# Kernel optimization log

Measured on AMD Instinct MI355X. Metric: run time of the kernel, lower is better.

Reference implementation:

```python
import jax, jax.numpy as jnp
import numpy as np

N, C, HEADS = 32768, 512, 8
CK = CV = C // 2   # key/value channels (= hidden//2 per AE.block1)
F2 = C // 2        # CAM in_features
BN_EPS = 1e-5


def _bn(x, p):
    # eval-mode BatchNorm2d on [n, c, w] (h=1 squeezed); p = [gamma, beta, mean, var] each [c]
    g, b, m, v = p
    inv = g / jnp.sqrt(v + BN_EPS)
    return (x - m[None, :, None]) * inv[None, :, None] + b[None, :, None]


def _conv(x, w):
    # 1x1 Conv2d (no bias) on [n, c, w]; w: [out_c, in_c]
    return jnp.einsum('ncw,oc->now', x, w)


def _block(x, y, ea_wk, ea_bk, ea_wq, ea_bq, ea_wv, ea_bv, ea_wr, ea_br,
           pool_w1, pool_bn1, pool_w2, pool_bn2,
           adapt_w1, adapt_bn1, adapt_w2, adapt_bn2,
           delta_w1, delta_bn1, delta_w2):
    # torch: input_ = stack([x, y]).permute([0,2,1]).unsqueeze(2) -> [2, C, 1, N]; we drop h=1 -> [2, C, N]
    inp = jnp.stack([x, y]).transpose(0, 2, 1)  # [2, C, N]

    # ---------------- EfficientAttention ----------------
    keys = _conv(inp, ea_wk) + ea_bk[None, :, None]      # [2, CK, N]
    queries = _conv(inp, ea_wq) + ea_bq[None, :, None]   # [2, CK, N]
    values = _conv(inp, ea_wv) + ea_bv[None, :, None]    # [2, CV, N]
    hk, hv = CK // HEADS, CV // HEADS
    K = jax.nn.softmax(keys.reshape(2, HEADS, hk, N), axis=-1)     # softmax over positions
    Q = jax.nn.softmax(queries.reshape(2, HEADS, hk, N), axis=2)   # softmax over head channels
    V = values.reshape(2, HEADS, hv, N)
    ctx = jnp.einsum('nhkw,nhvw->nhkv', K, V)                      # [2, H, hk, hv]
    att = jnp.einsum('nhkv,nhkw->nhvw', ctx, Q).reshape(2, CV, N)  # [2, CV, N]
    ea_full = _conv(att, ea_wr) + ea_br[None, :, None] + inp       # reprojection + residual
    ea_out = ((ea_full[0] + ea_full[1]) * 0.5).T                   # [N, C]

    # ---------------- CAM ----------------
    high = inp.mean(axis=2, keepdims=True)                 # AdaptiveAvgPool2d(1) -> [2, C, 1]
    high = _bn(_conv(high, pool_w1), pool_bn1)
    high = _bn(_conv(high, pool_w2), pool_bn2)             # [2, F2, 1]
    low = _bn(_conv(inp, adapt_w1), adapt_bn1)
    low = _bn(_conv(low, adapt_w2), adapt_bn2)             # [2, F2, N]
    # bilinear upsample of a 1x1 map == broadcast
    high_up = jnp.broadcast_to(high, (2, F2, N))
    concat = jnp.concatenate([low, high_up], axis=1)       # [2, 2*F2, N]
    d = _bn(_conv(concat, delta_w1), delta_bn1)
    delta = _conv(d, delta_w2)                             # [2, 2, N]: (dx, dy)
    # grid_sample of 1x1 `high`, zeros padding, align_corners=False; norm = [w/s, h/s] = [1, 1]
    gx = jnp.linspace(-1.0, 1.0, N)[None, :] + delta[:, 0]  # h_list + delta_x, [2, N]
    gy = -1.0 + delta[:, 1]                                 # linspace(-1,1,1) = -1
    ix, iy = gx * 0.5, gy * 0.5                             # unnormalized coords for W=H=1
    wgt = jnp.clip(1.0 - jnp.abs(ix), 0.0, 1.0) * jnp.clip(1.0 - jnp.abs(iy), 0.0, 1.0)  # [2, N]
    sampled = high * wgt[:, None, :]                        # [2, F2, N]
    cam_full = jnp.concatenate([sampled, low], axis=1)      # [2, 2*F2, N] == [2, C, N]
    cam_out = ((cam_full[0] + cam_full[1]) * 0.5).T         # [N, C]

    return (ea_out + cam_out) * 0.5                         # [N, C]


def setup_inputs() -> dict:
    key = jax.random.key(0)
    ks = iter(jax.random.split(key, 40))
    def rn(shape, s=0.05):
        return jax.random.normal(next(ks), shape, jnp.float32) * s
    def bn(c):
        p = jax.random.normal(next(ks), (4, c), jnp.float32) * 0.05
        p = p.at[0].add(1.0)                 # gamma ~ 1
        p = p.at[3].set(jnp.abs(p[3]) + 1.0)  # var > 0
        return p
    return {
        'x': jax.random.normal(next(ks), (N, C), jnp.float32),
        'y': jax.random.normal(next(ks), (N, C), jnp.float32),
        'ea_wk': rn((CK, C)), 'ea_bk': rn((CK,)),
        'ea_wq': rn((CK, C)), 'ea_bq': rn((CK,)),
        'ea_wv': rn((CV, C)), 'ea_bv': rn((CV,)),
        'ea_wr': rn((C, CV)), 'ea_br': rn((C,)),
        'pool_w1': rn((C, C)), 'pool_bn1': bn(C),
        'pool_w2': rn((F2, C)), 'pool_bn2': bn(F2),
        'adapt_w1': rn((C, C)), 'adapt_bn1': bn(C),
        'adapt_w2': rn((F2, C)), 'adapt_bn2': bn(F2),
        'delta_w1': rn((F2, 2 * F2)), 'delta_bn1': bn(F2),
        'delta_w2': rn((2, F2)),
    }


def reference(x, y, ea_wk, ea_bk, ea_wq, ea_bq, ea_wv, ea_bv, ea_wr, ea_br,
              pool_w1, pool_bn1, pool_w2, pool_bn2,
              adapt_w1, adapt_bn1, adapt_w2, adapt_bn2,
              delta_w1, delta_bn1, delta_w2):
    return _block(x, y, ea_wk, ea_bk, ea_wq, ea_bq, ea_wv, ea_bv, ea_wr, ea_br,
                  pool_w1, pool_bn1, pool_w2, pool_bn2,
                  adapt_w1, adapt_bn1, adapt_w2, adapt_bn2,
                  delta_w1, delta_bn1, delta_w2)
```

## Files before the change

### kernel.cpp

```cpp
#include <hip/hip_runtime.h>
#include <math.h>

#define B_CTXC   0
#define B_ZP     524288
#define B_COLS   526336
#define B_HIGH2  530432
#define B_CONSTD 532480
#define B_BIASO  532544
#define B_CPP    534592
#define B_CTXT   535616
#define B_WDD    568384
#define B_WDX    570432
#define B_WL     574528
#define B_WBIG   1098816
#define B_WKV    1639488
#define B_WR     2163776
#define B_PW1T   2425920
#define B_PW2T   3474496
#define B_D1BT   3998784

typedef __attribute__((ext_vector_type(8))) short bf16x8;
typedef __attribute__((ext_vector_type(4))) float f32x4;

#define MFMA(a, b, c) __builtin_amdgcn_mfma_f32_16x16x32_bf16(a, b, c, 0, 0, 0)
#define EVSWZ(row) ((((row) >> 1) & 3) << 4)

__device__ inline unsigned f2bfu(float f) {
  unsigned u = __float_as_uint(f);
  return (u + 0x7FFFu + ((u >> 16) & 1u)) >> 16;
}
__device__ inline unsigned pack2(float a, float b) { return f2bfu(a) | (f2bfu(b) << 16); }

__device__ inline void softmax_pack(f32x4 a0, f32x4 a1, const float* __restrict__ bq,
                                    int hh, int g, unsigned o[4]) {
  float q[8], e[8];
  float mx = -1e30f;
#pragma unroll
  for (int r = 0; r < 4; ++r) {
    q[r] = a0[r] + bq[hh * 32 + g * 4 + r];
    q[4 + r] = a1[r] + bq[hh * 32 + 16 + g * 4 + r];
    mx = fmaxf(mx, fmaxf(q[r], q[4 + r]));
  }
  mx = fmaxf(mx, __shfl_xor(mx, 16, 64));
  mx = fmaxf(mx, __shfl_xor(mx, 32, 64));
  float sm = 0.f;
#pragma unroll
  for (int r = 0; r < 8; ++r) { e[r] = __expf(q[r] - mx); sm += e[r]; }
  sm += __shfl_xor(sm, 16, 64);
  sm += __shfl_xor(sm, 32, 64);
  float inv = 1.f / sm;
  o[0] = pack2(e[0] * inv, e[1] * inv); o[1] = pack2(e[2] * inv, e[3] * inv);
  o[2] = pack2(e[4] * inv, e[5] * inv); o[3] = pack2(e[6] * inv, e[7] * inv);
}

__global__ __launch_bounds__(512) void kFuse1(
    const float* __restrict__ a1, const float* __restrict__ abn1,
    const float* __restrict__ a2, const float* __restrict__ abn2,
    const float* __restrict__ wq, const float* __restrict__ wk, const float* __restrict__ wv,
    const float* __restrict__ wr, const float* __restrict__ pw1, const float* __restrict__ pw2,
    const float* __restrict__ d1, char* __restrict__ wsb) {
  __shared__ float S1[512], F1[512], redu[512];
  const int t = threadIdx.x;
  float* wsf = (float*)wsb;
  unsigned short* u16 = (unsigned short*)wsb;
  if (blockIdx.x < 256) {
    const int o = blockIdx.x;
    {
      float gg = abn1[t], be = abn1[512 + t], mn = abn1[1024 + t], va = abn1[1536 + t];
      float s = gg * rsqrtf(va + 1e-5f);
      S1[t] = s; F1[t] = be - mn * s;
    }
    float g2 = abn2[o], be2 = abn2[256 + o], mn2 = abn2[512 + o], va2 = abn2[768 + o];
    float s2 = g2 * rsqrtf(va2 + 1e-5f);
    float f2v = be2 - mn2 * s2;
    __syncthreads();
    float acc = 0.f;
    const float* a2r = a2 + o * 512;
    for (int m = 0; m < 512; ++m) acc = fmaf(a2r[m] * S1[m], a1[m * 512 + t], acc);
    wsf[(B_WL / 4) + o * 512 + t] = s2 * acc;
    redu[t] = a2r[t] * F1[t];
    __syncthreads();
    for (int sft = 256; sft >= 1; sft >>= 1) {
      if (t < sft) redu[t] += redu[t + sft];
      __syncthreads();
    }
    if (t == 0) wsf[(B_CPP / 4) + o] = s2 * redu[0] + f2v;
    return;
  }
  int i = (blockIdx.x - 256) * 512 + t;
  if (i < 131072) {
    int T = i >> 13, r = i & 8191;
    int ks = r >> 9, l = (r >> 3) & 63, j = r & 7;
    int row = T * 16 + (l & 15);
    int col = ks * 32 + (l >> 4) * 8 + j;
    u16[(B_WBIG / 2) + i] = (unsigned short)f2bfu(wq[row * 512 + col]);
    return;
  }
  i -= 131072;
  if (i < 262144) {
    int T = i >> 13, r = i & 8191;
    int ks = r >> 9, l = (r >> 3) & 63, j = r & 7;
    int row = T * 16 + (l & 15);
    int col = ks * 32 + (l >> 4) * 8 + j;
    float v = row < 256 ? wk[row * 512 + col] : wv[(row - 256) * 512 + col];
    u16[(B_WKV / 2) + i] = (unsigned short)f2bfu(v);
    return;
  }
  i -= 262144;
  if (i < 131072) {
    int T = i >> 12, r = i & 4095;
    int ks = r >> 9, l = (r >> 3) & 63, j = r & 7;
    int row = T * 16 + (l & 15);
    int col = ks * 32 + (l >> 4) * 8 + j;
    u16[(B_WR / 2) + i] = (unsigned short)f2bfu(wr[row * 256 + col]);
    return;
  }
  i -= 131072;
  if (i < 262144) { int o = i >> 9, c = i & 511; wsf[(B_PW1T / 4) + c * 512 + o] = pw1[i]; return; }
  i -= 262144;
  if (i < 131072) { int o = i >> 9, c = i & 511; wsf[(B_PW2T / 4) + c * 256 + o] = pw2[i]; return; }
  i -= 131072;
  if (i < 65536) { int o = i >> 8, v = i & 255; wsf[(B_D1BT / 4) + v * 256 + o] = d1[o * 512 + 256 + v]; }
}

__global__ __launch_bounds__(512) void kW2(
    const float* __restrict__ d1, const float* __restrict__ dbn1,
    const float* __restrict__ d2, char* __restrict__ wsb) {
  __shared__ float SD[256], WDDl[512], part[512];
  const int t = threadIdx.x, blk = blockIdx.x;
  float* wsf = (float*)wsb;
  if (t < 256) {
    float gg = dbn1[t], va = dbn1[768 + t];
    SD[t] = gg * rsqrtf(va + 1e-5f);
  }
  __syncthreads();
  {
    int j = t >> 8, v = t & 255;
    float acc = 0.f;
    for (int o = 0; o < 256; ++o) acc = fmaf(d2[j * 256 + o] * SD[o], d1[o * 512 + v], acc);
    WDDl[t] = acc;
    if (blk == 0) wsf[(B_WDD / 4) + t] = acc;
  }
  __syncthreads();
  const int cl = t & 63, vp = t >> 6;
  const int c = blk * 64 + cl;
  float acc0 = 0.f, acc1 = 0.f;
  for (int v = vp * 32; v < vp * 32 + 32; ++v) {
    float wl = wsf[(B_WL / 4) + v * 512 + c];
    acc0 = fmaf(WDDl[v], wl, acc0);
    acc1 = fmaf(WDDl[256 + v], wl, acc1);
  }
  part[t] = acc0;
  __syncthreads();
  if (t < 64) {
    float s = 0.f;
#pragma unroll
    for (int p2 = 0; p2 < 8; ++p2) s += part[p2 * 64 + t];
    wsf[(B_WDX / 4) + blk * 64 + t] = s;
  }
  __syncthreads();
  part[t] = acc1;
  __syncthreads();
  if (t < 64) {
    float s = 0.f;
#pragma unroll
    for (int p2 = 0; p2 < 8; ++p2) s += part[p2 * 64 + t];
    wsf[(B_WDX / 4) + 512 + blk * 64 + t] = s;
  }
}

__global__ __launch_bounds__(512) void kPackB(char* __restrict__ wsb) {
  float* wsf = (float*)wsb;
  unsigned short* u16 = (unsigned short*)wsb;
  int i = blockIdx.x * 512 + threadIdx.x + 131072;
  if (i >= 270336) return;
  int T = i >> 13, r = i & 8191;
  int ks = r >> 9, l = (r >> 3) & 63, j = r & 7;
  int row = T * 16 + (l & 15);
  int col = ks * 32 + (l >> 4) * 8 + j;
  float v;
  if (row < 512) v = wsf[(B_WL / 4) + (row - 256) * 512 + col];
  else if (row < 514) v = wsf[(B_WDX / 4) + (row - 512) * 512 + col];
  else v = 0.f;
  u16[(B_WBIG / 2) + i] = (unsigned short)f2bfu(v);
}

__global__ __launch_bounds__(1024, 2) void k1_reduce(
    const float* __restrict__ x, const float* __restrict__ y,
    const float* __restrict__ bk, const float* __restrict__ bv,
    const char* __restrict__ wsb, float* __restrict__ outp) {
  __shared__ __align__(16) unsigned char XYl[65536];
  __shared__ float Red[1536];
  unsigned char* Xl = XYl;
  unsigned char* Yl = XYl + 32768;
  float* PSf = (float*)XYl;
  unsigned char* elx = XYl;
  unsigned char* ely = XYl + 16384;
  unsigned char* vlx = XYl + 32768;
  unsigned char* vly = XYl + 49152;
  const int t = threadIdx.x;
  const int tw = t >> 6, lo16 = t & 15, g = (t >> 4) & 3, l = t & 63;
  const char* Wkv = wsb + B_WKV;

  if (t < 512) Red[t] = 0.f;
  float csum[2][8];
#pragma unroll
  for (int b2 = 0; b2 < 2; ++b2)
#pragma unroll
    for (int i = 0; i < 8; ++i) csum[b2][i] = 0.f;
  const int n0 = blockIdx.x * 32;
  const int bbase0 = lo16 * 1024 + g * 16;
  const int bbase1 = bbase0 + 16384;
  const int bswz = (lo16 & 7) << 4;
  const int pp0 = lo16, pp1 = 16 + lo16;

#pragma unroll
  for (int r = 0; r < 2; ++r) {
    int chunk = r * 1024 + t;
    int prow = chunk >> 6, j = chunk & 63;
    const f32x4* gx = (const f32x4*)(x + (size_t)(n0 + prow) * 512 + j * 8);
    const f32x4* gy = (const f32x4*)(y + (size_t)(n0 + prow) * 512 + j * 8);
    f32x4 x0 = __builtin_nontemporal_load(gx);
    f32x4 x1 = __builtin_nontemporal_load(gx + 1);
    f32x4 y0 = __builtin_nontemporal_load(gy);
    f32x4 y1 = __builtin_nontemporal_load(gy + 1);
#pragma unroll
    for (int q2 = 0; q2 < 4; ++q2) {
      csum[0][q2] += x0[q2]; csum[0][4 + q2] += x1[q2];
      csum[1][q2] += y0[q2]; csum[1][4 + q2] += y1[q2];
    }
    int byte = (prow * 1024 + j * 16) ^ ((prow & 7) << 4);
    uint4 pk;
    pk.x = pack2(x0[0], x0[1]); pk.y = pack2(x0[2], x0[3]);
    pk.z = pack2(x1[0], x1[1]); pk.w = pack2(x1[2], x1[3]);
    *(uint4*)(Xl + byte) = pk;
    pk.x = pack2(y0[0], y0[1]); pk.y = pack2(y0[2], y0[3]);
    pk.z = pack2(y1[0], y1[1]); pk.w = pack2(y1[2], y1[3]);
    *(uint4*)(Yl + byte) = pk;
  }
  __syncthreads();

  f32x4 ax0p0 = {0,0,0,0}, ax0p1 = {0,0,0,0}, ay0p0 = {0,0,0,0}, ay0p1 = {0,0,0,0};
  f32x4 ax1p0 = {0,0,0,0}, ax1p1 = {0,0,0,0}, ay1p0 = {0,0,0,0}, ay1p1 = {0,0,0,0};
  {
    int t0 = tw * 2;
    const char* ap = Wkv + t0 * 16384 + l * 16;
    __builtin_amdgcn_s_setprio(1);
#pragma unroll
    for (int ks = 0; ks < 16; ++ks) {
      bf16x8 bx0 = *(const bf16x8*)(Xl + ((bbase0 + ks * 64) ^ bswz));
      bf16x8 bx1 = *(const bf16x8*)(Xl + ((bbase1 + ks * 64) ^ bswz));
      bf16x8 by0 = *(const bf16x8*)(Yl + ((bbase0 + ks * 64) ^ bswz));
      bf16x8 by1 = *(const bf16x8*)(Yl + ((bbase1 + ks * 64) ^ bswz));
      bf16x8 af0 = *(const bf16x8*)(ap + ks * 1024);
      bf16x8 af1 = *(const bf16x8*)(ap + 16384 + ks * 1024);
      ax0p0 = MFMA(af0, bx0, ax0p0); ax0p1 = MFMA(af0, bx1, ax0p1);
      ay0p0 = MFMA(af0, by0, ay0p0); ay0p1 = MFMA(af0, by1, ay0p1);
      ax1p0 = MFMA(af1, bx0, ax1p0); ax1p1 = MFMA(af1, bx1, ax1p1);
      ay1p0 = MFMA(af1, by0, ay1p0); ay1p1 = MFMA(af1, by1, ay1p1);
    }
    __builtin_amdgcn_s_setprio(0);
  }
  float ex0[2][4], ex1[2][4], ey0[2][4], ey1[2][4];
  if (tw < 8) {
    int t0 = tw * 2, t1 = t0 + 1;
#pragma unroll
    for (int pt2 = 0; pt2 < 2; ++pt2) {
      f32x4 Ax0 = pt2 ? ax0p1 : ax0p0, Ax1 = pt2 ? ax1p1 : ax1p0;
      f32x4 Ay0 = pt2 ? ay0p1 : ay0p0, Ay1 = pt2 ? ay1p1 : ay1p0;
#pragma unroll
      for (int r = 0; r < 4; ++r) {
        float bk0 = bk[t0 * 16 + g * 4 + r], bk1 = bk[t1 * 16 + g * 4 + r];
        ex0[pt2][r] = __expf(Ax0[r] + bk0); ey0[pt2][r] = __expf(Ay0[r] + bk0);
        ex1[pt2][r] = __expf(Ax1[r] + bk1); ey1[pt2][r] = __expf(Ay1[r] + bk1);
      }
#pragma unroll
      for (int r = 0; r < 4; ++r) {
        float v0 = ex0[pt2][r], v1 = ex1[pt2][r], v2 = ey0[pt2][r], v3 = ey1[pt2][r];
        for (int m = 8; m >= 1; m >>= 1) {
          v0 += __shfl_xor(v0, m, 16); v1 += __shfl_xor(v1, m, 16);
          v2 += __shfl_xor(v2, m, 16); v3 += __shfl_xor(v3, m, 16);
        }
        if (lo16 == 0) {
          atomicAdd(&Red[t0 * 16 + g * 4 + r], v0);
          atomicAdd(&Red[t1 * 16 + g * 4 + r], v1);
          atomicAdd(&Red[256 + t0 * 16 + g * 4 + r], v2);
          atomicAdd(&Red[256 + t1 * 16 + g * 4 + r], v3);
        }
      }
    }
  }
  __syncthreads();

#pragma unroll
  for (int b = 0; b < 2; ++b)
#pragma unroll
    for (int i = 0; i < 8; ++i) PSf[t * 16 + b * 8 + i] = csum[b][i];
  __syncthreads();
  {
    int s = t, b = s >> 9, ch = s & 511, tlow = ch >> 3, ii = ch & 7;
    float sum = 0.f;
#pragma unroll
    for (int w2 = 0; w2 < 16; ++w2) sum += PSf[(w2 * 64 + tlow) * 16 + b * 8 + ii];
    Red[512 + s] = sum;
  }
  __syncthreads();

  if (tw < 8) {
    int t0 = tw * 2, t1 = t0 + 1;
#pragma unroll
    for (int pt2 = 0; pt2 < 2; ++pt2) {
      int pp = pt2 ? pp1 : pp0;
#pragma unroll
      for (int r = 0; r < 4; ++r) {
        int row0 = t0 * 16 + g * 4 + r;
        int row1 = t1 * 16 + g * 4 + r;
        int a0 = (row0 * 64 + pp * 2) ^ EVSWZ(row0);
        int a1 = (row1 * 64 + pp * 2) ^ EVSWZ(row1);
        *(unsigned short*)(elx + a0) = (unsigned short)f2bfu(ex0[pt2][r]);
        *(unsigned short*)(elx + a1) = (unsigned short)f2bfu(ex1[pt2][r]);
        *(unsigned short*)(ely + a0) = (unsigned short)f2bfu(ey0[pt2][r]);
        *(unsigned short*)(ely + a1) = (unsigned short)f2bfu(ey1[pt2][r]);
      }
    }
  } else {
    int t0 = tw * 2, t1 = t0 + 1;
#pragma unroll
    for (int pt2 = 0; pt2 < 2; ++pt2) {
      f32x4 Ax0 = pt2 ? ax0p1 : ax0p0, Ax1 = pt2 ? ax1p1 : ax1p0;
      f32x4 Ay0 = pt2 ? ay0p1 : ay0p0, Ay1 = pt2 ? ay1p1 : ay1p0;
      int pp = pt2 ? pp1 : pp0;
#pragma unroll
      for (int r = 0; r < 4; ++r) {
        int row0 = (t0 - 16) * 16 + g * 4 + r;
        int row1 = (t1 - 16) * 16 + g * 4 + r;
        float bv0 = bv[row0], bv1 = bv[row1];
        int a0 = (row0 * 64 + pp * 2) ^ EVSWZ(row0);
        int a1 = (row1 * 64 + pp * 2) ^ EVSWZ(row1);
        *(unsigned short*)(vlx + a0) = (unsigned short)f2bfu(Ax0[r] + bv0);
        *(unsigned short*)(vlx + a1) = (unsigned short)f2bfu(Ax1[r] + bv1);
        *(unsigned short*)(vly + a0) = (unsigned short)f2bfu(Ay0[r] + bv0);
        *(unsigned short*)(vly + a1) = (unsigned short)f2bfu(Ay1[r] + bv1);
      }
    }
  }
  __syncthreads();

  {
    const int h2 = tw & 7, bsel = tw >> 3;
    const unsigned char* el = bsel ? ely : elx;
    const unsigned char* vl = bsel ? vly : vlx;
    unsigned* ctxp = (unsigned*)outp + (size_t)blockIdx.x * 8192;
#pragma unroll
    for (int m = 0; m < 2; ++m) {
      int rowe = h2 * 32 + m * 16 + lo16;
      bf16x8 ea = *(const bf16x8*)(el + ((rowe * 64 + g * 16) ^ EVSWZ(rowe)));
      f32x4 c0 = {0.f, 0.f, 0.f, 0.f}, c1 = {0.f, 0.f, 0.f, 0.f};
      {
        int rowv = h2 * 32 + lo16;
        bf16x8 vb = *(const bf16x8*)(vl + ((rowv * 64 + g * 16) ^ EVSWZ(rowv)));
        c0 = MFMA(ea, vb, c0);
      }
      {
        int rowv = h2 * 32 + 16 + lo16;
        bf16x8 vb = *(const bf16x8*)(vl + ((rowv * 64 + g * 16) ^ EVSWZ(rowv)));
        c1 = MFMA(ea, vb, c1);
      }
#pragma unroll
      for (int r = 0; r < 4; ++r)
        __builtin_nontemporal_store(pack2(c0[r], c1[r]),
            &ctxp[((bsel * 2 + m) * 4 + r) * 512 + h2 * 64 + l]);
    }
    float* redp = outp + 8388608 + blockIdx.x * 1536;
    for (int i = t; i < 1536; i += 1024) __builtin_nontemporal_store(Red[i], &redp[i]);
  }
}

__global__ __launch_bounds__(512) void k1b(const float* __restrict__ outp, char* __restrict__ wsb) {
  __shared__ float R[512];
  const int t = threadIdx.x, blk = blockIdx.x;
  float* wsf = (float*)wsb;
  if (blk < 128) {
    int sl = t & 63, part = t >> 6;
    int slot = blk * 64 + sl;
    const unsigned* p = (const unsigned*)outp;
    float s0 = 0.f, s1 = 0.f;
    for (int c = part * 128; c < part * 128 + 128; ++c) {
      unsigned wv = __builtin_nontemporal_load(&p[(size_t)c * 8192 + slot]);
      s0 += __uint_as_float(wv << 16);
      s1 += __uint_as_float(wv & 0xffff0000u);
    }
    R[sl * 8 + part] = s0;
    __syncthreads();
    float sum0 = 0.f;
#pragma unroll
    for (int p2 = 0; p2 < 8; ++p2) sum0 += R[sl * 8 + p2];
    __syncthreads();
    R[sl * 8 + part] = s1;
    __syncthreads();
    float sum1 = 0.f;
#pragma unroll
    for (int p2 = 0; p2 < 8; ++p2) sum1 += R[sl * 8 + p2];
    if (part == 0) {
      int t_ = slot & 511, bmr = slot >> 9;
      int r = bmr & 3, m = (bmr >> 2) & 1, b = bmr >> 3;
      int h = t_ >> 6, g = (t_ >> 4) & 3, lo16 = t_ & 15;
      int klocal = m * 16 + g * 4 + r;
      int base = ((b * 8 + h) * 32 + klocal) * 32;
      wsf[(B_CTXC / 4) + base + lo16] = sum0;
      wsf[(B_CTXC / 4) + base + 16 + lo16] = sum1;
    }
  } else {
    int sj = t & 15, part = t >> 4;
    int slot = (blk - 128) * 16 + sj;
    const float* rp = outp + 8388608;
    float s = 0.f;
    for (int cc = part * 32; cc < part * 32 + 32; ++cc)
      s += __builtin_nontemporal_load(&rp[(size_t)cc * 1536 + slot]);
    R[t] = s;
    __syncthreads();
    if (t < 16) {
      float sum = 0.f;
#pragma unroll
      for (int p2 = 0; p2 < 32; ++p2) sum += R[t + p2 * 16];
      int j = (blk - 128) * 16 + t;
      if (j < 512) wsf[(B_ZP / 4) + j] = sum;
      else wsf[(B_COLS / 4) + (j - 512)] = sum;
    }
  }
}

__global__ __launch_bounds__(512) void k2_finalize(
    const float* __restrict__ pbn1, const float* __restrict__ pbn2,
    const float* __restrict__ dbn1, const float* __restrict__ d2,
    const float* __restrict__ ea_br, char* __restrict__ wsb) {
  __shared__ float HI[1024], H1[1024], H2l[512], VB[512], slot[4];
  const int t = threadIdx.x;
  float* wsf = (float*)wsb;
  unsigned short* u16 = (unsigned short*)wsb;
  if (blockIdx.x < 32) {
    int idx = blockIdx.x * 512 + t;
    float s = wsf[(B_CTXC / 4) + idx];
    int v = idx & 31, row = idx >> 5;
    int b = row >> 8, kr = row & 255;
    int hh = kr >> 5, kh = kr & 31;
    float val = s / wsf[(B_ZP / 4) + b * 256 + kr];
    int m = v >> 4;
    int lane = (v & 15) + ((kh >> 3) << 4);
    int j = kh & 7;
    u16[(B_CTXT / 2) + (((b * 8 + hh) * 2 + m) << 9) + lane * 8 + j] = (unsigned short)f2bfu(val);
    return;
  }
  if (t < 4) slot[t] = 0.f;
  for (int idx = t; idx < 1024; idx += 512) HI[idx] = wsf[(B_COLS / 4) + idx] * (1.f / 32768.f);
  __syncthreads();
  {
    int o = t;
    float gg = pbn1[o], be = pbn1[512 + o], mn = pbn1[1024 + o], va = pbn1[1536 + o];
    float sc = gg * rsqrtf(va + 1e-5f), sh = be - mn * sc;
    for (int b = 0; b < 2; ++b) {
      float acc = 0.f;
      for (int c = 0; c < 512; ++c) acc = fmaf(wsf[(B_PW1T / 4) + c * 512 + o], HI[b * 512 + c], acc);
      H1[b * 512 + o] = acc * sc + sh;
    }
  }
  __syncthreads();
  if (t < 256) {
    int o = t;
    float gg = pbn2[o], be = pbn2[256 + o], mn = pbn2[512 + o], va = pbn2[768 + o];
    float sc = gg * rsqrtf(va + 1e-5f), sh = be - mn * sc;
    for (int b = 0; b < 2; ++b) {
      float acc = 0.f;
      for (int c = 0; c < 512; ++c) acc = fmaf(wsf[(B_PW2T / 4) + c * 256 + o], H1[b * 512 + c], acc);
      float vv = acc * sc + sh;
      H2l[b * 256 + o] = vv;
      wsf[(B_HIGH2 / 4) + b * 256 + o] = vv;
    }
  }
  __syncthreads();
  if (t < 256) {
    int o = t;
    float gg = dbn1[o], be = dbn1[256 + o], mn = dbn1[512 + o], va = dbn1[768 + o];
    float sd = gg * rsqrtf(va + 1e-5f), fd = be - mn * sd;
    for (int b = 0; b < 2; ++b) {
      float acc = 0.f;
      for (int v = 0; v < 256; ++v) acc = fmaf(wsf[(B_D1BT / 4) + v * 256 + o], H2l[b * 256 + v], acc);
      VB[b * 256 + o] = sd * acc + fd;
    }
  }
  __syncthreads();
  if (t < 256) {
    int o = t;
    for (int b = 0; b < 2; ++b)
      for (int j = 0; j < 2; ++j) atomicAdd(&slot[b * 2 + j], d2[j * 256 + o] * VB[b * 256 + o]);
    float cp = wsf[(B_CPP / 4) + o];
    for (int j = 0; j < 2; ++j) {
      float w = wsf[(B_WDD / 4) + j * 256 + o] * cp;
      atomicAdd(&slot[0 + j], w);
      atomicAdd(&slot[2 + j], w);
    }
  }
  __syncthreads();
  if (t < 4) wsf[(B_CONSTD / 4) + t] = slot[t];
  {
    int o = t;
    float bb = 0.5f * ea_br[o];
    if (o >= 256) bb += 0.5f * wsf[(B_CPP / 4) + o - 256];
    wsf[(B_BIASO / 4) + o] = bb;
  }
}

__global__ __launch_bounds__(1024, 1) void k3_main(
    const float* __restrict__ x, const float* __restrict__ y,
    const float* __restrict__ bq, const char* __restrict__ wsb,
    float* __restrict__ out) {
  __shared__ __align__(16) unsigned char Xl[32768];
  __shared__ __align__(16) unsigned char Yl[32768];
  __shared__ __align__(16) unsigned char ACCb[65536];
  __shared__ __align__(16) unsigned char Ql[16384];
  __shared__ float wgtl[64];
  const int t = threadIdx.x;
  const int tw = t >> 6, lo16 = t & 15, g = (t >> 4) & 3, l = t & 63;
  const int n0 = blockIdx.x * 32;
  const char* Wbig = wsb + B_WBIG;
  const char* WRp = wsb + B_WR;
  const char* CTXT = wsb + B_CTXT;
  const float* wsf = (const float*)wsb;
  const int bbase0 = lo16 * 1024 + g * 16;
  const int bbase1 = bbase0 + 16384;
  const int bswz = (lo16 & 7) << 4;
  const int swzq = (lo16 & 7) << 4;

#pragma unroll
  for (int r = 0; r < 2; ++r) {
    int chunk = r * 1024 + t;
    int prow = chunk >> 6, j = chunk & 63;
    const f32x4* gx = (const f32x4*)(x + (size_t)(n0 + prow) * 512 + j * 8);
    const f32x4* gy = (const f32x4*)(y + (size_t)(n0 + prow) * 512 + j * 8);
    f32x4 x0 = __builtin_nontemporal_load(gx);
    f32x4 x1 = __builtin_nontemporal_load(gx + 1);
    f32x4 y0 = __builtin_nontemporal_load(gy);
    f32x4 y1 = __builtin_nontemporal_load(gy + 1);
    int byte = (prow * 1024 + j * 16) ^ ((prow & 7) << 4);
    uint4 pk;
    pk.x = pack2(x0[0], x0[1]); pk.y = pack2(x0[2], x0[3]);
    pk.z = pack2(x1[0], x1[1]); pk.w = pack2(x1[2], x1[3]);
    *(uint4*)(Xl + byte) = pk;
    pk.x = pack2(y0[0], y0[1]); pk.y = pack2(y0[2], y0[3]);
    pk.z = pack2(y1[0], y1[1]); pk.w = pack2(y1[2], y1[3]);
    *(uint4*)(Yl + byte) = pk;
    int abase = prow * 2048 + j * 32;
    int aswz = (prow & 7) << 4;
    f32x4 a0 = 0.25f * (x0 + y0);
    f32x4 a1 = 0.25f * (x1 + y1);
    *(f32x4*)(ACCb + (abase ^ aswz)) = a0;
    *(f32x4*)(ACCb + ((abase + 16) ^ aswz)) = a1;
  }
  __syncthreads();

  f32x4 ax0p0 = {0,0,0,0}, ax0p1 = {0,0,0,0}, ay0p0 = {0,0,0,0}, ay0p1 = {0,0,0,0};
  f32x4 ax1p0 = {0,0,0,0}, ax1p1 = {0,0,0,0}, ay1p0 = {0,0,0,0}, ay1p1 = {0,0,0,0};
  {
    int t0 = tw * 2;
    const char* ap = Wbig + t0 * 16384 + l * 16;
    __builtin_amdgcn_s_setprio(1);
#pragma unroll
    for (int ks = 0; ks < 16; ++ks) {
      bf16x8 bx0 = *(const bf16x8*)(Xl + ((bbase0 + ks * 64) ^ bswz));
      bf16x8 bx1 = *(const bf16x8*)(Xl + ((bbase1 + ks * 64) ^ bswz));
      bf16x8 by0 = *(const bf16x8*)(Yl + ((bbase0 + ks * 64) ^ bswz));
      bf16x8 by1 = *(const bf16x8*)(Yl + ((bbase1 + ks * 64) ^ bswz));
      bf16x8 af0 = *(const bf16x8*)(ap + ks * 1024);
      bf16x8 af1 = *(const bf16x8*)(ap + 16384 + ks * 1024);
      ax0p0 = MFMA(af0, bx0, ax0p0); ax0p1 = MFMA(af0, bx1, ax0p1);
      ay0p0 = MFMA(af0, by0, ay0p0); ay0p1 = MFMA(af0, by1, ay0p1);
      ax1p0 = MFMA(af1, bx0, ax1p0); ax1p1 = MFMA(af1, bx1, ax1p1);
      ay1p0 = MFMA(af1, by0, ay1p0); ay1p1 = MFMA(af1, by1, ay1p1);
    }
    __builtin_amdgcn_s_setprio(0);
  }

  unsigned Qy0[4], Qy1[4];

  if (tw < 8) {
    int hh = tw;
    unsigned o[4];
    softmax_pack(ax0p0, ax1p0, bq, hh, g, o);
    {
      int base_q = lo16 * 512 + hh * 64 + g * 8;
      uint2 w0; w0.x = o[0]; w0.y = o[1];
      uint2 w1; w1.x = o[2]; w1.y = o[3];
      *(uint2*)(Ql + (base_q ^ swzq)) = w0;
      *(uint2*)(Ql + ((base_q + 32) ^ swzq)) = w1;
    }
    softmax_pack(ay0p0, ay1p0, bq, hh, g, Qy0);
    softmax_pack(ax0p1, ax1p1, bq, hh, g, o);
    {
      int base_q = lo16 * 512 + hh * 64 + g * 8;
      uint2 w0; w0.x = o[0]; w0.y = o[1];
      uint2 w1; w1.x = o[2]; w1.y = o[3];
      *(uint2*)(Ql + 8192 + (base_q ^ swzq)) = w0;
      *(uint2*)(Ql + 8192 + ((base_q + 32) ^ swzq)) = w1;
    }
    softmax_pack(ay0p1, ay1p1, bq, hh, g, Qy1);
  } else {
    int tile0 = tw * 2 - 16;
#pragma unroll
    for (int pt2 = 0; pt2 < 2; ++pt2) {
      int row = pt2 * 16 + lo16;
      int rsw = (row & 7) << 4;
#pragma unroll
      for (int half = 0; half < 2; ++half) {
        f32x4 axs = half ? (pt2 ? ax1p1 : ax1p0) : (pt2 ? ax0p1 : ax0p0);
        f32x4 ays = half ? (pt2 ? ay1p1 : ay1p0) : (pt2 ? ay0p1 : ay0p0);
        int ch4 = 64 + (tile0 + half) * 4 + g;
        int ab = (row * 2048 + ch4 * 16) ^ rsw;
        f32x4 cur = *(const f32x4*)(ACCb + ab);
        cur += 0.25f * (axs + ays);
        *(f32x4*)(ACCb + ab) = cur;
      }
    }
  }

  if (tw == 15) {
    f32x4 adxp0 = {0,0,0,0}, adxp1 = {0,0,0,0}, adyp0 = {0,0,0,0}, adyp1 = {0,0,0,0};
    const char* ap = Wbig + 32 * 16384 + l * 16;
#pragma unroll
    for (int ks = 0; ks < 16; ++ks) {
      bf16x8 bx0 = *(const bf16x8*)(Xl + ((bbase0 + ks * 64) ^ bswz));
      bf16x8 bx1 = *(const bf16x8*)(Xl + ((bbase1 + ks * 64) ^ bswz));
      bf16x8 by0 = *(const bf16x8*)(Yl + ((bbase0 + ks * 64) ^ bswz));
      bf16x8 by1 = *(const bf16x8*)(Yl + ((bbase1 + ks * 64) ^ bswz));
      bf16x8 af = *(const bf16x8*)(ap + ks * 1024);
      adxp0 = MFMA(af, bx0, adxp0); adxp1 = MFMA(af, bx1, adxp1);
      adyp0 = MFMA(af, by0, adyp0); adyp1 = MFMA(af, by1, adyp1);
    }
    if (g == 0) {
#pragma unroll
      for (int pt2 = 0; pt2 < 2; ++pt2) {
        int pos = n0 + pt2 * 16 + lo16;
        float base_gx = -1.f + 2.f * (float)pos / 32767.f;
#pragma unroll
        for (int b = 0; b < 2; ++b) {
          f32x4 ad = b ? (pt2 ? adyp1 : adyp0) : (pt2 ? adxp1 : adxp0);
          float d0 = ad[0] + wsf[(B_CONSTD / 4) + b * 2 + 0];
          float d1 = ad[1] + wsf[(B_CONSTD / 4) + b * 2 + 1];
          float gxv = base_gx + d0;
          float gyv = -1.f + d1;
          float ix = gxv * 0.5f, iy = gyv * 0.5f;
          float wx = fminf(fmaxf(1.f - fabsf(ix), 0.f), 1.f);
          float wy = fminf(fmaxf(1.f - fabsf(iy), 0.f), 1.f);
          wgtl[b * 32 + pt2 * 16 + lo16] = wx * wy;
        }
      }
    }
  }

  if (tw < 8) {
    int hh = tw;
#pragma unroll
    for (int pt2 = 0; pt2 < 2; ++pt2) {
      unsigned char* Qs = Ql + pt2 * 8192;
      const unsigned* Qy = pt2 ? Qy1 : Qy0;
      f32x4 at0 = {0,0,0,0}, at1 = {0,0,0,0};
      {
        bf16x8 qf = *(const bf16x8*)(Qs + ((lo16 * 512 + hh * 64 + g * 16) ^ swzq));
        const char* cp = CTXT + (0 * 8 + hh) * 2048 + l * 16;
        bf16x8 c0 = *(const bf16x8*)(cp);
        bf16x8 c1 = *(const bf16x8*)(cp + 1024);
        at0 = MFMA(c0, qf, at0);
        at1 = MFMA(c1, qf, at1);
      }
      {
        int base_q = lo16 * 512 + hh * 64 + g * 8;
        uint2 w0; w0.x = Qy[0]; w0.y = Qy[1];
        uint2 w1; w1.x = Qy[2]; w1.y = Qy[3];
        *(uint2*)(Qs + (base_q ^ swzq)) = w0;
        *(uint2*)(Qs + ((base_q + 32) ^ swzq)) = w1;
      }
      {
        bf16x8 qf = *(const bf16x8*)(Qs + ((lo16 * 512 + hh * 64 + g * 16) ^ swzq));
        const char* cp = CTXT + (1 * 8 + hh) * 2048 + l * 16;
        bf16x8 c0 = *(const bf16x8*)(cp);
        bf16x8 c1 = *(const bf16x8*)(cp + 1024);
        at0 = MFMA(c0, qf, at0);
        at1 = MFMA(c1, qf, at1);
      }
#pragma unroll
      for (int m = 0; m < 2; ++m) {
        f32x4 v = m ? at1 : at0;
        uint2 wv;
        wv.x = pack2(v[0], v[1]); wv.y = pack2(v[2], v[3]);
        int byte = (lo16 * 512 + hh * 64 + m * 32 + g * 8) ^ swzq;
        *(uint2*)(Qs + byte) = wv;
      }
    }
  }
  __syncthreads();

  {
    int T0 = tw * 2;
    f32x4 r0p0 = {0,0,0,0}, r0p1 = {0,0,0,0}, r1p0 = {0,0,0,0}, r1p1 = {0,0,0,0};
    const char* ap = WRp + T0 * 8192 + l * 16;
    __builtin_amdgcn_s_setprio(1);
#pragma unroll
    for (int ks = 0; ks < 8; ++ks) {
      bf16x8 br0 = *(const bf16x8*)(Ql + ((lo16 * 512 + g * 16 + ks * 64) ^ swzq));
      bf16x8 br1 = *(const bf16x8*)(Ql + 8192 + ((lo16 * 512 + g * 16 + ks * 64) ^ swzq));
      bf16x8 a0 = *(const bf16x8*)(ap + ks * 1024);
      bf16x8 a1 = *(const bf16x8*)(ap + 8192 + ks * 1024);
      r0p0 = MFMA(a0, br0, r0p0); r0p1 = MFMA(a0, br1, r0p1);
      r1p0 = MFMA(a1, br0, r1p0); r1p1 = MFMA(a1, br1, r1p1);
    }
    __builtin_amdgcn_s_setprio(0);
#pragma unroll
    for (int pt2 = 0; pt2 < 2; ++pt2) {
      int row = pt2 * 16 + lo16;
      int rsw = (row & 7) << 4;
#pragma unroll
      for (int half = 0; half < 2; ++half) {
        f32x4 rr = half ? (pt2 ? r1p1 : r1p0) : (pt2 ? r0p1 : r0p0);
        int ch4 = (T0 + half) * 4 + g;
        int ab = (row * 2048 + ch4 * 16) ^ rsw;
        f32x4 cur = *(const f32x4*)(ACCb + ab);
        cur += 0.25f * rr;
        *(f32x4*)(ACCb + ab) = cur;
      }
    }
  }
  __syncthreads();

  const float* bo = wsf + (B_BIASO / 4);
#pragma unroll
  for (int i = 0; i < 4; ++i) {
    int idx = i * 1024 + t;
    int pos = idx >> 7, c4 = idx & 127;
    int ab = (pos * 2048 + c4 * 16) ^ ((pos & 7) << 4);
    f32x4 acc = *(const f32x4*)(ACCb + ab);
    f32x4 bb = *(const f32x4*)(bo + c4 * 4);
    if (c4 < 64) {
      f32x4 h20 = *(const f32x4*)(wsf + (B_HIGH2 / 4) + c4 * 4);
      f32x4 h21 = *(const f32x4*)(wsf + (B_HIGH2 / 4) + 256 + c4 * 4);
      float wg0 = wgtl[pos], wg1 = wgtl[32 + pos];
      acc += (0.25f * wg0) * h20 + (0.25f * wg1) * h21;
    }
    acc += bb;
    __builtin_nontemporal_store(acc, (f32x4*)(out + (size_t)(n0 + pos) * 512 + c4 * 4));
  }
}

extern "C" void kernel_launch(void* const* d_in, const int* in_sizes, int n_in,
                              void* d_out, int out_size, void* d_ws, size_t ws_size,
                              hipStream_t stream) {
  const float* x = (const float*)d_in[0];
  const float* y = (const float*)d_in[1];
  const float* ea_wk = (const float*)d_in[2];
  const float* ea_bk = (const float*)d_in[3];
  const float* ea_wq = (const float*)d_in[4];
  const float* ea_bq = (const float*)d_in[5];
  const float* ea_wv = (const float*)d_in[6];
  const float* ea_bv = (const float*)d_in[7];
  const float* ea_wr = (const float*)d_in[8];
  const float* ea_br = (const float*)d_in[9];
  const float* pool_w1 = (const float*)d_in[10];
  const float* pool_bn1 = (const float*)d_in[11];
  const float* pool_w2 = (const float*)d_in[12];
  const float* pool_bn2 = (const float*)d_in[13];
  const float* adapt_w1 = (const float*)d_in[14];
  const float* adapt_bn1 = (const float*)d_in[15];
  const float* adapt_w2 = (const float*)d_in[16];
  const float* adapt_bn2 = (const float*)d_in[17];
  const float* delta_w1 = (const float*)d_in[18];
  const float* delta_bn1 = (const float*)d_in[19];
  const float* delta_w2 = (const float*)d_in[20];
  char* ws = (char*)d_ws;
  float* out = (float*)d_out;

  kFuse1<<<2176, 512, 0, stream>>>(adapt_w1, adapt_bn1, adapt_w2, adapt_bn2,
                                   ea_wq, ea_wk, ea_wv, ea_wr, pool_w1, pool_w2,
                                   delta_w1, ws);
  kW2<<<8, 512, 0, stream>>>(delta_w1, delta_bn1, delta_w2, ws);
  kPackB<<<272, 512, 0, stream>>>(ws);
  k1_reduce<<<1024, 1024, 0, stream>>>(x, y, ea_bk, ea_bv, ws, out);
  k1b<<<224, 512, 0, stream>>>(out, ws);
  k2_finalize<<<33, 512, 0, stream>>>(pool_bn1, pool_bn2, delta_bn1, delta_w2, ea_br, ws);
  k3_main<<<1024, 1024, 0, stream>>>(x, y, ea_bq, ws, out);
}
```

Baseline: 304.9 us.

## Halve k3_main position tile to 16 to double grid size and occupancy

Each k3_main block now handles 16 positions instead of 32. Per-block LDS drops from about 144KB to about 72KB and the per-wave accumulator count is halved, and the grid doubles to 2048 blocks. The aim is to fit more blocks per CU and hide memory latency better. In exchange, every weight fragment (Wbig, WR, CTXT) read from global or L2 is reused across half as many positions, so weight traffic per output doubles.

```diff
diff --git a/kernel.cpp b/kernel.cpp
--- a/kernel.cpp
+++ b/kernel.cpp
@@ -510,31 +510,28 @@
   }
 }
 
-__global__ __launch_bounds__(1024, 1) void k3_main(
+__global__ __launch_bounds__(1024, 8) void k3_main(
     const float* __restrict__ x, const float* __restrict__ y,
     const float* __restrict__ bq, const char* __restrict__ wsb,
     float* __restrict__ out) {
-  __shared__ __align__(16) unsigned char Xl[32768];
-  __shared__ __align__(16) unsigned char Yl[32768];
-  __shared__ __align__(16) unsigned char ACCb[65536];
-  __shared__ __align__(16) unsigned char Ql[16384];
-  __shared__ float wgtl[64];
+  __shared__ __align__(16) unsigned char Xl[16384];
+  __shared__ __align__(16) unsigned char Yl[16384];
+  __shared__ __align__(16) unsigned char ACCb[32768];
+  __shared__ __align__(16) unsigned char Ql[8192];
+  __shared__ float wgtl[32];
   const int t = threadIdx.x;
   const int tw = t >> 6, lo16 = t & 15, g = (t >> 4) & 3, l = t & 63;
-  const int n0 = blockIdx.x * 32;
+  const int n0 = blockIdx.x * 16;
   const char* Wbig = wsb + B_WBIG;
   const char* WRp = wsb + B_WR;
   const char* CTXT = wsb + B_CTXT;
   const float* wsf = (const float*)wsb;
   const int bbase0 = lo16 * 1024 + g * 16;
-  const int bbase1 = bbase0 + 16384;
   const int bswz = (lo16 & 7) << 4;
   const int swzq = (lo16 & 7) << 4;
 
-#pragma unroll
-  for (int r = 0; r < 2; ++r) {
-    int chunk = r * 1024 + t;
-    int prow = chunk >> 6, j = chunk & 63;
+  {
+    int prow = t >> 6, j = t & 63;
     const f32x4* gx = (const f32x4*)(x + (size_t)(n0 + prow) * 512 + j * 8);
     const f32x4* gy = (const f32x4*)(y + (size_t)(n0 + prow) * 512 + j * 8);
     f32x4 x0 = __builtin_nontemporal_load(gx);
@@ -558,8 +555,7 @@
   }
   __syncthreads();
 
-  f32x4 ax0p0 = {0,0,0,0}, ax0p1 = {0,0,0,0}, ay0p0 = {0,0,0,0}, ay0p1 = {0,0,0,0};
-  f32x4 ax1p0 = {0,0,0,0}, ax1p1 = {0,0,0,0}, ay1p0 = {0,0,0,0}, ay1p1 = {0,0,0,0};
+  f32x4 axT0 = {0,0,0,0}, ayT0 = {0,0,0,0}, axT1 = {0,0,0,0}, ayT1 = {0,0,0,0};
   {
     int t0 = tw * 2;
     const char* ap = Wbig + t0 * 16384 + l * 16;
@@ -567,25 +563,21 @@
 #pragma unroll
     for (int ks = 0; ks < 16; ++ks) {
       bf16x8 bx0 = *(const bf16x8*)(Xl + ((bbase0 + ks * 64) ^ bswz));
-      bf16x8 bx1 = *(const bf16x8*)(Xl + ((bbase1 + ks * 64) ^ bswz));
       bf16x8 by0 = *(const bf16x8*)(Yl + ((bbase0 + ks * 64) ^ bswz));
-      bf16x8 by1 = *(const bf16x8*)(Yl + ((bbase1 + ks * 64) ^ bswz));
       bf16x8 af0 = *(const bf16x8*)(ap + ks * 1024);
       bf16x8 af1 = *(const bf16x8*)(ap + 16384 + ks * 1024);
-      ax0p0 = MFMA(af0, bx0, ax0p0); ax0p1 = MFMA(af0, bx1, ax0p1);
-      ay0p0 = MFMA(af0, by0, ay0p0); ay0p1 = MFMA(af0, by1, ay0p1);
-      ax1p0 = MFMA(af1, bx0, ax1p0); ax1p1 = MFMA(af1, bx1, ax1p1);
-      ay1p0 = MFMA(af1, by0, ay1p0); ay1p1 = MFMA(af1, by1, ay1p1);
+      axT0 = MFMA(af0, bx0, axT0); ayT0 = MFMA(af0, by0, ayT0);
+      axT1 = MFMA(af1, bx0, axT1); ayT1 = MFMA(af1, by0, ayT1);
     }
     __builtin_amdgcn_s_setprio(0);
   }
 
-  unsigned Qy0[4], Qy1[4];
+  unsigned Qy[4];
 
   if (tw < 8) {
     int hh = tw;
     unsigned o[4];
-    softmax_pack(ax0p0, ax1p0, bq, hh, g, o);
+    softmax_pack(axT0, axT1, bq, hh, g, o);
     {
       int base_q = lo16 * 512 + hh * 64 + g * 8;
       uint2 w0; w0.x = o[0]; w0.y = o[1];
@@ -593,146 +585,116 @@
       *(uint2*)(Ql + (base_q ^ swzq)) = w0;
       *(uint2*)(Ql + ((base_q + 32) ^ swzq)) = w1;
     }
-    softmax_pack(ay0p0, ay1p0, bq, hh, g, Qy0);
-    softmax_pack(ax0p1, ax1p1, bq, hh, g, o);
+    softmax_pack(ayT0, ayT1, bq, hh, g, Qy);
+  } else {
+    int tile0 = tw * 2 - 16;
+    int row = lo16, rsw = (row & 7) << 4;
+#pragma unroll
+    for (int half = 0; half < 2; ++half) {
+      f32x4 axs = half ? axT1 : axT0;
+      f32x4 ays = half ? ayT1 : ayT0;
+      int ch4 = 64 + (tile0 + half) * 4 + g;
+      int ab = (row * 2048 + ch4 * 16) ^ rsw;
+      f32x4 cur = *(const f32x4*)(ACCb + ab);
+      cur += 0.25f * (axs + ays);
+      *(f32x4*)(ACCb + ab) = cur;
+    }
+  }
+
+  if (tw == 15) {
+    f32x4 adx = {0,0,0,0}, ady = {0,0,0,0};
+    const char* ap = Wbig + 32 * 16384 + l * 16;
+#pragma unroll
+    for (int ks = 0; ks < 16; ++ks) {
+      bf16x8 bx0 = *(const bf16x8*)(Xl + ((bbase0 + ks * 64) ^ bswz));
+      bf16x8 by0 = *(const bf16x8*)(Yl + ((bbase0 + ks * 64) ^ bswz));
+      bf16x8 af = *(const bf16x8*)(ap + ks * 1024);
+      adx = MFMA(af, bx0, adx); ady = MFMA(af, by0, ady);
+    }
+    if (g == 0) {
+      int pos = n0 + lo16;
+      float base_gx = -1.f + 2.f * (float)pos / 32767.f;
+#pragma unroll
+      for (int b = 0; b < 2; ++b) {
+        f32x4 ad = b ? ady : adx;
+        float d0 = ad[0] + wsf[(B_CONSTD / 4) + b * 2 + 0];
+        float d1 = ad[1] + wsf[(B_CONSTD / 4) + b * 2 + 1];
+        float gxv = base_gx + d0;
+        float gyv = -1.f + d1;
+        float ix = gxv * 0.5f, iy = gyv * 0.5f;
+        float wx = fminf(fmaxf(1.f - fabsf(ix), 0.f), 1.f);
+        float wy = fminf(fmaxf(1.f - fabsf(iy), 0.f), 1.f);
+        wgtl[b * 16 + lo16] = wx * wy;
+      }
+    }
+  }
+
+  if (tw < 8) {
+    int hh = tw;
+    f32x4 at0 = {0,0,0,0}, at1 = {0,0,0,0};
+    {
+      bf16x8 qf = *(const bf16x8*)(Ql + ((lo16 * 512 + hh * 64 + g * 16) ^ swzq));
+      const char* cp = CTXT + (0 * 8 + hh) * 2048 + l * 16;
+      bf16x8 c0 = *(const bf16x8*)(cp);
+      bf16x8 c1 = *(const bf16x8*)(cp + 1024);
+      at0 = MFMA(c0, qf, at0);
+      at1 = MFMA(c1, qf, at1);
+    }
     {
       int base_q = lo16 * 512 + hh * 64 + g * 8;
-      uint2 w0; w0.x = o[0]; w0.y = o[1];
-      uint2 w1; w1.x = o[2]; w1.y = o[3];
-      *(uint2*)(Ql + 8192 + (base_q ^ swzq)) = w0;
-      *(uint2*)(Ql + 8192 + ((base_q + 32) ^ swzq)) = w1;
-    }
-    softmax_pack(ay0p1, ay1p1, bq, hh, g, Qy1);
-  } else {
-    int tile0 = tw * 2 - 16;
-#pragma unroll
-    for (int pt2 = 0; pt2 < 2; ++pt2) {
-      int row = pt2 * 16 + lo16;
-      int rsw = (row & 7) << 4;
-#pragma unroll
-      for (int half = 0; half < 2; ++half) {
-        f32x4 axs = half ? (pt2 ? ax1p1 : ax1p0) : (pt2 ? ax0p1 : ax0p0);
-        f32x4 ays = half ? (pt2 ? ay1p1 : ay1p0) : (pt2 ? ay0p1 : ay0p0);
-        int ch4 = 64 + (tile0 + half) * 4 + g;
-        int ab = (row * 2048 + ch4 * 16) ^ rsw;
-        f32x4 cur = *(const f32x4*)(ACCb + ab);
-        cur += 0.25f * (axs + ays);
-        *(f32x4*)(ACCb + ab) = cur;
-      }
-    }
-  }
-
-  if (tw == 15) {
-    f32x4 adxp0 = {0,0,0,0}, adxp1 = {0,0,0,0}, adyp0 = {0,0,0,0}, adyp1 = {0,0,0,0};
-    const char* ap = Wbig + 32 * 16384 + l * 16;
-#pragma unroll
-    for (int ks = 0; ks < 16; ++ks) {
-      bf16x8 bx0 = *(const bf16x8*)(Xl + ((bbase0 + ks * 64) ^ bswz));
-      bf16x8 bx1 = *(const bf16x8*)(Xl + ((bbase1 + ks * 64) ^ bswz));
-      bf16x8 by0 = *(const bf16x8*)(Yl + ((bbase0 + ks * 64) ^ bswz));
-      bf16x8 by1 = *(const bf16x8*)(Yl + ((bbase1 + ks * 64) ^ bswz));
-      bf16x8 af = *(const bf16x8*)(ap + ks * 1024);
-      adxp0 = MFMA(af, bx0, adxp0); adxp1 = MFMA(af, bx1, adxp1);
-      adyp0 = MFMA(af, by0, adyp0); adyp1 = MFMA(af, by1, adyp1);
-    }
-    if (g == 0) {
-#pragma unroll
-      for (int pt2 = 0; pt2 < 2; ++pt2) {
-        int pos = n0 + pt2 * 16 + lo16;
-        float base_gx = -1.f + 2.f * (float)pos / 32767.f;
-#pragma unroll
-        for (int b = 0; b < 2; ++b) {
-          f32x4 ad = b ? (pt2 ? adyp1 : adyp0) : (pt2 ? adxp1 : adxp0);
-          float d0 = ad[0] + wsf[(B_CONSTD / 4) + b * 2 + 0];
-          float d1 = ad[1] + wsf[(B_CONSTD / 4) + b * 2 + 1];
-          float gxv = base_gx + d0;
-          float gyv = -1.f + d1;
-          float ix = gxv * 0.5f, iy = gyv * 0.5f;
-          float wx = fminf(fmaxf(1.f - fabsf(ix), 0.f), 1.f);
-          float wy = fminf(fmaxf(1.f - fabsf(iy), 0.f), 1.f);
-          wgtl[b * 32 + pt2 * 16 + lo16] = wx * wy;
-        }
-      }
-    }
-  }
-
-  if (tw < 8) {
-    int hh = tw;
-#pragma unroll
-    for (int pt2 = 0; pt2 < 2; ++pt2) {
-      unsigned char* Qs = Ql + pt2 * 8192;
-      const unsigned* Qy = pt2 ? Qy1 : Qy0;
-      f32x4 at0 = {0,0,0,0}, at1 = {0,0,0,0};
-      {
-        bf16x8 qf = *(const bf16x8*)(Qs + ((lo16 * 512 + hh * 64 + g * 16) ^ swzq));
-        const char* cp = CTXT + (0 * 8 + hh) * 2048 + l * 16;
-        bf16x8 c0 = *(const bf16x8*)(cp);
-        bf16x8 c1 = *(const bf16x8*)(cp + 1024);
-        at0 = MFMA(c0, qf, at0);
-        at1 = MFMA(c1, qf, at1);
-      }
-      {
-        int base_q = lo16 * 512 + hh * 64 + g * 8;
-        uint2 w0; w0.x = Qy[0]; w0.y = Qy[1];
-        uint2 w1; w1.x = Qy[2]; w1.y = Qy[3];
-        *(uint2*)(Qs + (base_q ^ swzq)) = w0;
-        *(uint2*)(Qs + ((base_q + 32) ^ swzq)) = w1;
-      }
-      {
-        bf16x8 qf = *(const bf16x8*)(Qs + ((lo16 * 512 + hh * 64 + g * 16) ^ swzq));
-        const char* cp = CTXT + (1 * 8 + hh) * 2048 + l * 16;
-        bf16x8 c0 = *(const bf16x8*)(cp);
-        bf16x8 c1 = *(const bf16x8*)(cp + 1024);
-        at0 = MFMA(c0, qf, at0);
-        at1 = MFMA(c1, qf, at1);
-      }
-#pragma unroll
-      for (int m = 0; m < 2; ++m) {
-        f32x4 v = m ? at1 : at0;
-        uint2 wv;
-        wv.x = pack2(v[0], v[1]); wv.y = pack2(v[2], v[3]);
-        int byte = (lo16 * 512 + hh * 64 + m * 32 + g * 8) ^ swzq;
-        *(uint2*)(Qs + byte) = wv;
-      }
+      uint2 w0; w0.x = Qy[0]; w0.y = Qy[1];
+      uint2 w1; w1.x = Qy[2]; w1.y = Qy[3];
+      *(uint2*)(Ql + (base_q ^ swzq)) = w0;
+      *(uint2*)(Ql + ((base_q + 32) ^ swzq)) = w1;
+    }
+    {
+      bf16x8 qf = *(const bf16x8*)(Ql + ((lo16 * 512 + hh * 64 + g * 16) ^ swzq));
+      const char* cp = CTXT + (1 * 8 + hh) * 2048 + l * 16;
+      bf16x8 c0 = *(const bf16x8*)(cp);
+      bf16x8 c1 = *(const bf16x8*)(cp + 1024);
+      at0 = MFMA(c0, qf, at0);
+      at1 = MFMA(c1, qf, at1);
+    }
+#pragma unroll
+    for (int m = 0; m < 2; ++m) {
+      f32x4 v = m ? at1 : at0;
+      uint2 wv;
+      wv.x = pack2(v[0], v[1]); wv.y = pack2(v[2], v[3]);
+      int byte = (lo16 * 512 + hh * 64 + m * 32 + g * 8) ^ swzq;
+      *(uint2*)(Ql + byte) = wv;
     }
   }
   __syncthreads();
 
   {
     int T0 = tw * 2;
-    f32x4 r0p0 = {0,0,0,0}, r0p1 = {0,0,0,0}, r1p0 = {0,0,0,0}, r1p1 = {0,0,0,0};
+    f32x4 r0 = {0,0,0,0}, r1 = {0,0,0,0};
     const char* ap = WRp + T0 * 8192 + l * 16;
     __builtin_amdgcn_s_setprio(1);
 #pragma unroll
     for (int ks = 0; ks < 8; ++ks) {
       bf16x8 br0 = *(const bf16x8*)(Ql + ((lo16 * 512 + g * 16 + ks * 64) ^ swzq));
-      bf16x8 br1 = *(const bf16x8*)(Ql + 8192 + ((lo16 * 512 + g * 16 + ks * 64) ^ swzq));
       bf16x8 a0 = *(const bf16x8*)(ap + ks * 1024);
       bf16x8 a1 = *(const bf16x8*)(ap + 8192 + ks * 1024);
-      r0p0 = MFMA(a0, br0, r0p0); r0p1 = MFMA(a0, br1, r0p1);
-      r1p0 = MFMA(a1, br0, r1p0); r1p1 = MFMA(a1, br1, r1p1);
+      r0 = MFMA(a0, br0, r0); r1 = MFMA(a1, br0, r1);
     }
     __builtin_amdgcn_s_setprio(0);
-#pragma unroll
-    for (int pt2 = 0; pt2 < 2; ++pt2) {
-      int row = pt2 * 16 + lo16;
-      int rsw = (row & 7) << 4;
-#pragma unroll
-      for (int half = 0; half < 2; ++half) {
-        f32x4 rr = half ? (pt2 ? r1p1 : r1p0) : (pt2 ? r0p1 : r0p0);
-        int ch4 = (T0 + half) * 4 + g;
-        int ab = (row * 2048 + ch4 * 16) ^ rsw;
-        f32x4 cur = *(const f32x4*)(ACCb + ab);
-        cur += 0.25f * rr;
-        *(f32x4*)(ACCb + ab) = cur;
-      }
+    int row = lo16, rsw = (row & 7) << 4;
+#pragma unroll
+    for (int half = 0; half < 2; ++half) {
+      f32x4 rr = half ? r1 : r0;
+      int ch4 = (T0 + half) * 4 + g;
+      int ab = (row * 2048 + ch4 * 16) ^ rsw;
+      f32x4 cur = *(const f32x4*)(ACCb + ab);
+      cur += 0.25f * rr;
+      *(f32x4*)(ACCb + ab) = cur;
     }
   }
   __syncthreads();
 
   const float* bo = wsf + (B_BIASO / 4);
 #pragma unroll
-  for (int i = 0; i < 4; ++i) {
+  for (int i = 0; i < 2; ++i) {
     int idx = i * 1024 + t;
     int pos = idx >> 7, c4 = idx & 127;
     int ab = (pos * 2048 + c4 * 16) ^ ((pos & 7) << 4);
@@ -741,7 +703,7 @@
     if (c4 < 64) {
       f32x4 h20 = *(const f32x4*)(wsf + (B_HIGH2 / 4) + c4 * 4);
       f32x4 h21 = *(const f32x4*)(wsf + (B_HIGH2 / 4) + 256 + c4 * 4);
-      float wg0 = wgtl[pos], wg1 = wgtl[32 + pos];
+      float wg0 = wgtl[pos], wg1 = wgtl[16 + pos];
       acc += (0.25f * wg0) * h20 + (0.25f * wg1) * h21;
     }
     acc += bb;
@@ -784,5 +746,5 @@
   k1_reduce<<<1024, 1024, 0, stream>>>(x, y, ea_bk, ea_bv, ws, out);
   k1b<<<224, 512, 0, stream>>>(out, ws);
   k2_finalize<<<33, 512, 0, stream>>>(pool_bn1, pool_bn2, delta_bn1, delta_w2, ea_br, ws);
-  k3_main<<<1024, 1024, 0, stream>>>(x, y, ea_bq, ws, out);
-}
+  k3_main<<<2048, 1024, 0, stream>>>(x, y, ea_bq, ws, out);
+}
```

New measurement: 323.4 us. 6.0% more time.
